# Performance work log

Hardware: AMD Instinct MI355X
Metric: run time of the kernel (lower is better)

The kernel has to match this reference:

```python
import jax, jax.numpy as jnp
import numpy as np

IN_FEATURES = 256
N_HEADS = 4
N_HIDDEN = 128  # out_features, concat=False
SLOPE = 0.1
NEG_INF = -9e15


def setup_inputs() -> dict:
    key = jax.random.key(0)
    k1, k2, k3, k4 = jax.random.split(key, 4)
    N = 8192
    h = jax.random.normal(k1, (N, IN_FEATURES), dtype=jnp.float32)
    adj_mat = jax.random.randint(k2, (N, N), 0, 2, dtype=jnp.int32)
    # xavier_normal with gain=1.414
    std_W = 1.414 * (2.0 / (IN_FEATURES + N_HIDDEN * N_HEADS)) ** 0.5
    W = jax.random.normal(k3, (IN_FEATURES, N_HIDDEN * N_HEADS), dtype=jnp.float32) * std_W
    std_a = 1.414 * (2.0 / (2 * N_HIDDEN + 1)) ** 0.5
    a = jax.random.normal(k4, (N_HEADS, 2 * N_HIDDEN, 1), dtype=jnp.float32) * std_a
    return {"h": h, "adj_mat": adj_mat, "W": W, "a": a}


def reference(h, adj_mat, W, a):
    N = h.shape[0]
    # linear projection -> [H, N, d]
    ht = (h @ W).reshape(N, N_HEADS, N_HIDDEN).transpose(1, 0, 2)
    # dropout is identity (eval / p effectively 0), then LeakyReLU
    ht = jnp.where(ht >= 0, ht, SLOPE * ht)
    # additive attention scores: src[h,i] + tgt[h,j]
    src = jnp.einsum('hnd,hd->hn', ht, a[:, :N_HIDDEN, 0])  # [H, N]
    tgt = jnp.einsum('hnd,hd->hn', ht, a[:, N_HIDDEN:, 0])  # [H, N]
    e = src[:, :, None] + tgt[:, None, :]                   # [H, N, N]
    e = jnp.where(adj_mat[None, :, :] > 0, e, NEG_INF)
    attn = jax.nn.softmax(e, axis=-1)
    # weighted sum and mean over heads (concat=False)
    out = jnp.einsum('hnm,hmd->hnd', attn, ht).mean(axis=0)  # [N, d]
    return out
```

## Files before the change

kernel.cpp:

```cpp
#include <hip/hip_runtime.h>


typedef unsigned short u16;
typedef unsigned int u32;
using bf16x8 = __attribute__((ext_vector_type(8))) short;
using f32x4  = __attribute__((ext_vector_type(4))) float;

typedef const void __attribute__((address_space(1))) gas_void;
typedef void __attribute__((address_space(3))) las_void;
#define GLD16(g, l) __builtin_amdgcn_global_load_lds((gas_void*)(g), (las_void*)(l), 16, 0, 0)

__device__ __forceinline__ u16 f2bf(float f) {
  u32 u = __float_as_uint(f);
  return (u16)((u + 0x7FFFu + ((u >> 16) & 1u)) >> 16);
}
__device__ __forceinline__ float bf2f(u16 u) {
  return __uint_as_float(((u32)u) << 16);
}

__global__ void transpose_w(const float* __restrict__ W, float* __restrict__ Wt) {
  __shared__ float tile[32][33];
  int cb = blockIdx.x * 32, kb = blockIdx.y * 32;
  int tc = threadIdx.x & 31, tr = threadIdx.x >> 5;
  for (int p = 0; p < 32; p += 8)
    tile[tr + p][tc] = W[(size_t)(kb + tr + p) * 512 + cb + tc];
  __syncthreads();
  for (int p = 0; p < 32; p += 8)
    Wt[(size_t)(cb + tr + p) * 256 + kb + tc] = tile[tc][tr + p];
}

__global__ void ht_gemm(const float* __restrict__ h, const float* __restrict__ Wt,
                        u16* __restrict__ HT) {
  __shared__ __align__(16) u16 Abuf[128 * 40];
  __shared__ __align__(16) u16 Bbuf[128 * 40];
  int tid = threadIdx.x;
  int cb = blockIdx.x, rb = blockIdx.y;
  int r0 = rb * 128, c0 = cb * 128;
  int lane = tid & 63, wv = tid >> 6;
  int wr = wv >> 1, wc = wv & 1;
  int mrow = lane & 15, q = lane >> 4;
  int ch = tid & 7, m0 = tid >> 3;

  f32x4 acc[4][4];
#pragma unroll
  for (int i = 0; i < 4; i++)
#pragma unroll
    for (int j = 0; j < 4; j++) acc[i][j] = f32x4{0.f, 0.f, 0.f, 0.f};

  for (int kt = 0; kt < 256; kt += 32) {
    __syncthreads();
#pragma unroll
    for (int mp = 0; mp < 128; mp += 32) {
      int m = m0 + mp;
      float4 v = *(const float4*)(&h[(size_t)(r0 + m) * 256 + kt + ch * 4]);
      uint2 p;
      p.x = (u32)f2bf(v.x) | ((u32)f2bf(v.y) << 16);
      p.y = (u32)f2bf(v.z) | ((u32)f2bf(v.w) << 16);
      *(uint2*)(&Abuf[m * 40 + ch * 4]) = p;
      float4 u = *(const float4*)(&Wt[(size_t)(c0 + m) * 256 + kt + ch * 4]);
      uint2 r;
      r.x = (u32)f2bf(u.x) | ((u32)f2bf(u.y) << 16);
      r.y = (u32)f2bf(u.z) | ((u32)f2bf(u.w) << 16);
      *(uint2*)(&Bbuf[m * 40 + ch * 4]) = r;
    }
    __syncthreads();
    bf16x8 af[4], bfv[4];
#pragma unroll
    for (int i = 0; i < 4; i++)
      af[i] = *(const bf16x8*)(&Abuf[(wr * 64 + i * 16 + mrow) * 40 + q * 8]);
#pragma unroll
    for (int j = 0; j < 4; j++)
      bfv[j] = *(const bf16x8*)(&Bbuf[(wc * 64 + j * 16 + mrow) * 40 + q * 8]);
#pragma unroll
    for (int i = 0; i < 4; i++)
#pragma unroll
      for (int j = 0; j < 4; j++)
        acc[i][j] = __builtin_amdgcn_mfma_f32_16x16x32_bf16(af[i], bfv[j], acc[i][j], 0, 0, 0);
  }
#pragma unroll
  for (int i = 0; i < 4; i++)
#pragma unroll
    for (int j = 0; j < 4; j++)
#pragma unroll
      for (int r = 0; r < 4; r++) {
        int gi = r0 + wr * 64 + i * 16 + q * 4 + r;
        int gc = c0 + wc * 64 + j * 16 + mrow;
        float v = acc[i][j][r];
        v = v >= 0.f ? v : 0.1f * v;
        HT[(size_t)gi * 512 + gc] = f2bf(v);
      }
}

__global__ void build_yt(const u16* __restrict__ HT, const float* __restrict__ a,
                         u16* __restrict__ Yt) {
  __shared__ u16 sht[64][528];
  __shared__ float swv[64 * 4];
  __shared__ float sa[512];
  int t = threadIdx.x;
  int j0 = blockIdx.x * 64;
  for (int i = t; i < 512; i += 256) {
    int g = i >> 7, d = i & 127;
    sa[i] = a[g * 256 + 128 + d];
  }
#pragma unroll
  for (int p = 0; p < 16; ++p) {
    int el = t + 256 * p;
    int row = el >> 6, col8 = el & 63;
    *(uint4*)(&sht[row][col8 * 8]) = *(const uint4*)(&HT[(size_t)(j0 + row) * 512 + col8 * 8]);
  }
  __syncthreads();
  {
    int jl = t >> 2, g = t & 3;
    float acc = 0.f;
#pragma unroll
    for (int d8 = 0; d8 < 16; ++d8) {
      bf16x8 v = *(const bf16x8*)(&sht[jl][g * 128 + d8 * 8]);
#pragma unroll
      for (int u = 0; u < 8; ++u)
        acc += bf2f((u16)v[u]) * sa[g * 128 + d8 * 8 + u];
    }
    swv[jl * 4 + g] = __expf(acc);
  }
  __syncthreads();
  int oj = (t & 7) * 8, oc = t >> 3;
  for (int pass = 0; pass < 17; ++pass) {
    int c = pass * 32 + oc;
    if (c >= 528) break;
    u32 pk[4] = {0u, 0u, 0u, 0u};
    if (c < 512) {
      int g = c >> 7;
#pragma unroll
      for (int u = 0; u < 4; ++u) {
        int j = oj + 2 * u;
        float v0 = bf2f(sht[j][c]) * swv[j * 4 + g];
        float v1 = bf2f(sht[j + 1][c]) * swv[(j + 1) * 4 + g];
        pk[u] = (u32)f2bf(v0) | ((u32)f2bf(v1) << 16);
      }
    } else if (c < 516) {
      int g = c - 512;
#pragma unroll
      for (int u = 0; u < 4; ++u) {
        int j = oj + 2 * u;
        float v0 = swv[j * 4 + g];
        float v1 = swv[(j + 1) * 4 + g];
        pk[u] = (u32)f2bf(v0) | ((u32)f2bf(v1) << 16);
      }
    }
    *(uint4*)(&Yt[(size_t)c * 8192 + j0 + oj]) = make_uint4(pk[0], pk[1], pk[2], pk[3]);
  }
}

__global__ __launch_bounds__(256, 2) void adj_gemm(const int* __restrict__ adj,
                                                   const u16* __restrict__ Yt,
                                                   float* __restrict__ C,
                                                   float* __restrict__ S) {
  __shared__ __align__(16) u16 Abuf[2][64 * 32];
  __shared__ __align__(16) u16 Bbuf[2][512 * 32];
  __shared__ __align__(16) u16 Bden[2][16 * 32];
  int tid = threadIdx.x;
  int rb = blockIdx.x, kh = blockIdx.y;
  int r0 = rb * 64, k0 = kh * 2048;
  int lane = tid & 63, wv = tid >> 6;
  int mrow = lane & 15, q = lane >> 4;
  int qs = q ^ ((mrow >> 1) & 3);
  int am = tid >> 2, aq = tid & 3;
  int asw = am * 32 + ((aq ^ ((am >> 1) & 3)) * 8);
  const int* aptr = &adj[(size_t)(r0 + am) * 8192 + k0 + aq * 8];
  int brow = lane >> 2;
  int bq = (lane & 3) ^ ((lane >> 3) & 3);

  f32x4 acc[4][8];
#pragma unroll
  for (int i = 0; i < 4; i++)
#pragma unroll
    for (int j = 0; j < 8; j++) acc[i][j] = f32x4{0.f, 0.f, 0.f, 0.f};
  f32x4 accD[4];
#pragma unroll
  for (int i = 0; i < 4; i++) accD[i] = f32x4{0.f, 0.f, 0.f, 0.f};

  {
#pragma unroll
    for (int p = 0; p < 8; ++p)
      GLD16(&Yt[(size_t)(wv * 128 + p * 16 + brow) * 8192 + k0 + bq * 8],
            &Bbuf[0][(wv * 128 + p * 16) * 32]);
    if (wv == 0)
      GLD16(&Yt[(size_t)(512 + brow) * 8192 + k0 + bq * 8], &Bden[0][0]);
    int4 v0 = *(const int4*)(aptr);
    int4 v1 = *(const int4*)(aptr + 4);
    uint4 pk;
    pk.x = 16256u * ((u32)v0.x | ((u32)v0.y << 16));
    pk.y = 16256u * ((u32)v0.z | ((u32)v0.w << 16));
    pk.z = 16256u * ((u32)v1.x | ((u32)v1.y << 16));
    pk.w = 16256u * ((u32)v1.z | ((u32)v1.w << 16));
    *(uint4*)(&Abuf[0][asw]) = pk;
    __syncthreads();
  }

  int cur = 0;
  for (int t = 0; t < 63; ++t) {
    int nxt = cur ^ 1;
    int kt = k0 + (t + 1) * 32;
#pragma unroll
    for (int p = 0; p < 8; ++p)
      GLD16(&Yt[(size_t)(wv * 128 + p * 16 + brow) * 8192 + kt + bq * 8],
            &Bbuf[nxt][(wv * 128 + p * 16) * 32]);
    if (wv == 0)
      GLD16(&Yt[(size_t)(512 + brow) * 8192 + kt + bq * 8], &Bden[nxt][0]);
    const int* ap = aptr + (size_t)(t + 1) * 32;
    int4 v0 = *(const int4*)(ap);
    int4 v1 = *(const int4*)(ap + 4);
    bf16x8 af[4], bfv[8];
#pragma unroll
    for (int i = 0; i < 4; i++)
      af[i] = *(const bf16x8*)(&Abuf[cur][(i * 16 + mrow) * 32 + qs * 8]);
#pragma unroll
    for (int j = 0; j < 8; j++)
      bfv[j] = *(const bf16x8*)(&Bbuf[cur][(wv * 128 + j * 16 + mrow) * 32 + qs * 8]);
#pragma unroll
    for (int i = 0; i < 4; i++)
#pragma unroll
      for (int j = 0; j < 8; j++)
        acc[i][j] = __builtin_amdgcn_mfma_f32_16x16x32_bf16(af[i], bfv[j], acc[i][j], 0, 0, 0);
    if (wv == 0) {
      bf16x8 bd = *(const bf16x8*)(&Bden[cur][mrow * 32 + qs * 8]);
#pragma unroll
      for (int i = 0; i < 4; i++)
        accD[i] = __builtin_amdgcn_mfma_f32_16x16x32_bf16(af[i], bd, accD[i], 0, 0, 0);
    }
    uint4 pk;
    pk.x = 16256u * ((u32)v0.x | ((u32)v0.y << 16));
    pk.y = 16256u * ((u32)v0.z | ((u32)v0.w << 16));
    pk.z = 16256u * ((u32)v1.x | ((u32)v1.y << 16));
    pk.w = 16256u * ((u32)v1.z | ((u32)v1.w << 16));
    *(uint4*)(&Abuf[nxt][asw]) = pk;
    __syncthreads();
    cur = nxt;
  }
  {
    bf16x8 af[4], bfv[8];
#pragma unroll
    for (int i = 0; i < 4; i++)
      af[i] = *(const bf16x8*)(&Abuf[cur][(i * 16 + mrow) * 32 + qs * 8]);
#pragma unroll
    for (int j = 0; j < 8; j++)
      bfv[j] = *(const bf16x8*)(&Bbuf[cur][(wv * 128 + j * 16 + mrow) * 32 + qs * 8]);
#pragma unroll
    for (int i = 0; i < 4; i++)
#pragma unroll
      for (int j = 0; j < 8; j++)
        acc[i][j] = __builtin_amdgcn_mfma_f32_16x16x32_bf16(af[i], bfv[j], acc[i][j], 0, 0, 0);
    if (wv == 0) {
      bf16x8 bd = *(const bf16x8*)(&Bden[cur][mrow * 32 + qs * 8]);
#pragma unroll
      for (int i = 0; i < 4; i++)
        accD[i] = __builtin_amdgcn_mfma_f32_16x16x32_bf16(af[i], bd, accD[i], 0, 0, 0);
    }
  }

  float* Ck = C + (size_t)kh * 8192 * 512;
#pragma unroll
  for (int i = 0; i < 4; i++)
#pragma unroll
    for (int j = 0; j < 8; j++)
#pragma unroll
      for (int r = 0; r < 4; r++) {
        int gi = r0 + i * 16 + q * 4 + r;
        int gc = wv * 128 + j * 16 + mrow;
        Ck[(size_t)gi * 512 + gc] = acc[i][j][r];
      }
  if (wv == 0 && mrow < 4) {
    float* Sk = S + (size_t)kh * 4 * 8192;
#pragma unroll
    for (int i = 0; i < 4; i++)
#pragma unroll
      for (int r = 0; r < 4; r++) {
        int gi = r0 + i * 16 + q * 4 + r;
        Sk[(size_t)mrow * 8192 + gi] = accD[i][r];
      }
  }
}

__global__ void finalize_gat(const float* __restrict__ C, const float* __restrict__ S,
                             float* __restrict__ out) {
  int idx = blockIdx.x * 256 + threadIdx.x;
  int i = idx >> 7, d = idx & 127;
  float s = 0.f;
#pragma unroll
  for (int g = 0; g < 4; ++g) {
    float num = 0.f, den = 0.f;
#pragma unroll
    for (int kh = 0; kh < 4; ++kh) {
      num += C[(size_t)kh * 8192 * 512 + (size_t)i * 512 + g * 128 + d];
      den += S[(size_t)kh * 4 * 8192 + (size_t)g * 8192 + i];
    }
    s += num / den;
  }
  out[idx] = 0.25f * s;
}

extern "C" void kernel_launch(void* const* d_in, const int* in_sizes, int n_in,
                              void* d_out, int out_size, void* d_ws, size_t ws_size,
                              hipStream_t stream) {
  const float* h   = (const float*)d_in[0];
  const int*   adj = (const int*)d_in[1];
  const float* W   = (const float*)d_in[2];
  const float* a   = (const float*)d_in[3];
  float* out = (float*)d_out;
  char* ws = (char*)d_ws;
  float* Wt = (float*)(ws + 0);
  u16*   HT = (u16*)(ws + 524288);
  u16*   Yt = (u16*)(ws + 8912896);
  float* C  = (float*)(ws + 17563648);
  float* S  = (float*)(ws + 84672512);

  transpose_w<<<dim3(16, 8), 256, 0, stream>>>(W, Wt);
  ht_gemm<<<dim3(4, 64), 256, 0, stream>>>(h, Wt, HT);
  build_yt<<<dim3(128), 256, 0, stream>>>(HT, a, Yt);
  adj_gemm<<<dim3(128, 4), 256, 0, stream>>>(adj, Yt, C, S);
  finalize_gat<<<dim3(4096), 256, 0, stream>>>(C, S, out);
}
```

Before: 509.1 us.

## Load GEMM B operand directly from global into registers, bypassing LDS staging

The adj_gemm kernel no longer stages the Yt B tiles and the denominator tile in double-buffered LDS through global_load_lds. Each wave now loads its own B fragments straight from global memory into registers, since no other wave reads them. Only the adjacency A tile stays in LDS, and the __syncthreads is replaced by an lgkmcnt wait plus s_barrier, so the barrier no longer waits on outstanding vector memory loads. This removes about 66KB of LDS per block and the LDS write/read round trip. In exchange, global load latency is no longer hidden by a one-tile-ahead prefetch, and the strided 64-byte row reads may coalesce less well.

Result: slower. 527.4 us (+3.6%).

```diff
diff --git a/kernel.cpp b/kernel.cpp
--- a/kernel.cpp
+++ b/kernel.cpp
@@ -5,10 +5,6 @@
 typedef unsigned int u32;
 using bf16x8 = __attribute__((ext_vector_type(8))) short;
 using f32x4  = __attribute__((ext_vector_type(4))) float;
-
-typedef const void __attribute__((address_space(1))) gas_void;
-typedef void __attribute__((address_space(3))) las_void;
-#define GLD16(g, l) __builtin_amdgcn_global_load_lds((gas_void*)(g), (las_void*)(l), 16, 0, 0)
 
 __device__ __forceinline__ u16 f2bf(float f) {
   u32 u = __float_as_uint(f);
@@ -155,8 +151,6 @@
                                                    float* __restrict__ C,
                                                    float* __restrict__ S) {
   __shared__ __align__(16) u16 Abuf[2][64 * 32];
-  __shared__ __align__(16) u16 Bbuf[2][512 * 32];
-  __shared__ __align__(16) u16 Bden[2][16 * 32];
   int tid = threadIdx.x;
   int rb = blockIdx.x, kh = blockIdx.y;
   int r0 = rb * 64, k0 = kh * 2048;
@@ -166,8 +160,8 @@
   int am = tid >> 2, aq = tid & 3;
   int asw = am * 32 + ((aq ^ ((am >> 1) & 3)) * 8);
   const int* aptr = &adj[(size_t)(r0 + am) * 8192 + k0 + aq * 8];
-  int brow = lane >> 2;
-  int bq = (lane & 3) ^ ((lane >> 3) & 3);
+  const u16* bbase = &Yt[(size_t)(wv * 128 + mrow) * 8192 + k0 + q * 8];
+  const u16* dbase = &Yt[(size_t)(512 + mrow) * 8192 + k0 + q * 8];
 
   f32x4 acc[4][8];
 #pragma unroll
@@ -179,12 +173,6 @@
   for (int i = 0; i < 4; i++) accD[i] = f32x4{0.f, 0.f, 0.f, 0.f};
 
   {
-#pragma unroll
-    for (int p = 0; p < 8; ++p)
-      GLD16(&Yt[(size_t)(wv * 128 + p * 16 + brow) * 8192 + k0 + bq * 8],
-            &Bbuf[0][(wv * 128 + p * 16) * 32]);
-    if (wv == 0)
-      GLD16(&Yt[(size_t)(512 + brow) * 8192 + k0 + bq * 8], &Bden[0][0]);
     int4 v0 = *(const int4*)(aptr);
     int4 v1 = *(const int4*)(aptr + 4);
     uint4 pk;
@@ -193,68 +181,49 @@
     pk.z = 16256u * ((u32)v1.x | ((u32)v1.y << 16));
     pk.w = 16256u * ((u32)v1.z | ((u32)v1.w << 16));
     *(uint4*)(&Abuf[0][asw]) = pk;
-    __syncthreads();
-  }
-
-  int cur = 0;
-  for (int t = 0; t < 63; ++t) {
-    int nxt = cur ^ 1;
-    int kt = k0 + (t + 1) * 32;
-#pragma unroll
-    for (int p = 0; p < 8; ++p)
-      GLD16(&Yt[(size_t)(wv * 128 + p * 16 + brow) * 8192 + kt + bq * 8],
-            &Bbuf[nxt][(wv * 128 + p * 16) * 32]);
-    if (wv == 0)
-      GLD16(&Yt[(size_t)(512 + brow) * 8192 + kt + bq * 8], &Bden[nxt][0]);
-    const int* ap = aptr + (size_t)(t + 1) * 32;
-    int4 v0 = *(const int4*)(ap);
-    int4 v1 = *(const int4*)(ap + 4);
-    bf16x8 af[4], bfv[8];
+  }
+  asm volatile("s_waitcnt lgkmcnt(0)" ::: "memory");
+  __builtin_amdgcn_s_barrier();
+
+  for (int t = 0; t < 64; ++t) {
+    int cur = t & 1;
+    size_t koff = (size_t)t * 32;
+    bf16x8 bfv[8];
+#pragma unroll
+    for (int j = 0; j < 8; j++)
+      bfv[j] = *(const bf16x8*)(bbase + (size_t)j * 16 * 8192 + koff);
+    bf16x8 bd;
+    if (wv == 0) bd = *(const bf16x8*)(dbase + koff);
+    int4 v0, v1;
+    if (t < 63) {
+      const int* ap = aptr + (size_t)(t + 1) * 32;
+      v0 = *(const int4*)(ap);
+      v1 = *(const int4*)(ap + 4);
+    }
+    bf16x8 af[4];
 #pragma unroll
     for (int i = 0; i < 4; i++)
       af[i] = *(const bf16x8*)(&Abuf[cur][(i * 16 + mrow) * 32 + qs * 8]);
 #pragma unroll
     for (int j = 0; j < 8; j++)
-      bfv[j] = *(const bf16x8*)(&Bbuf[cur][(wv * 128 + j * 16 + mrow) * 32 + qs * 8]);
-#pragma unroll
-    for (int i = 0; i < 4; i++)
-#pragma unroll
-      for (int j = 0; j < 8; j++)
+#pragma unroll
+      for (int i = 0; i < 4; i++)
         acc[i][j] = __builtin_amdgcn_mfma_f32_16x16x32_bf16(af[i], bfv[j], acc[i][j], 0, 0, 0);
     if (wv == 0) {
-      bf16x8 bd = *(const bf16x8*)(&Bden[cur][mrow * 32 + qs * 8]);
 #pragma unroll
       for (int i = 0; i < 4; i++)
         accD[i] = __builtin_amdgcn_mfma_f32_16x16x32_bf16(af[i], bd, accD[i], 0, 0, 0);
     }
-    uint4 pk;
-    pk.x = 16256u * ((u32)v0.x | ((u32)v0.y << 16));
-    pk.y = 16256u * ((u32)v0.z | ((u32)v0.w << 16));
-    pk.z = 16256u * ((u32)v1.x | ((u32)v1.y << 16));
-    pk.w = 16256u * ((u32)v1.z | ((u32)v1.w << 16));
-    *(uint4*)(&Abuf[nxt][asw]) = pk;
-    __syncthreads();
-    cur = nxt;
-  }
-  {
-    bf16x8 af[4], bfv[8];
-#pragma unroll
-    for (int i = 0; i < 4; i++)
-      af[i] = *(const bf16x8*)(&Abuf[cur][(i * 16 + mrow) * 32 + qs * 8]);
-#pragma unroll
-    for (int j = 0; j < 8; j++)
-      bfv[j] = *(const bf16x8*)(&Bbuf[cur][(wv * 128 + j * 16 + mrow) * 32 + qs * 8]);
-#pragma unroll
-    for (int i = 0; i < 4; i++)
-#pragma unroll
-      for (int j = 0; j < 8; j++)
-        acc[i][j] = __builtin_amdgcn_mfma_f32_16x16x32_bf16(af[i], bfv[j], acc[i][j], 0, 0, 0);
-    if (wv == 0) {
-      bf16x8 bd = *(const bf16x8*)(&Bden[cur][mrow * 32 + qs * 8]);
-#pragma unroll
-      for (int i = 0; i < 4; i++)
-        accD[i] = __builtin_amdgcn_mfma_f32_16x16x32_bf16(af[i], bd, accD[i], 0, 0, 0);
-    }
+    if (t < 63) {
+      uint4 pk;
+      pk.x = 16256u * ((u32)v0.x | ((u32)v0.y << 16));
+      pk.y = 16256u * ((u32)v0.z | ((u32)v0.w << 16));
+      pk.z = 16256u * ((u32)v1.x | ((u32)v1.y << 16));
+      pk.w = 16256u * ((u32)v1.z | ((u32)v1.w << 16));
+      *(uint4*)(&Abuf[cur ^ 1][asw]) = pk;
+    }
+    asm volatile("s_waitcnt lgkmcnt(0)" ::: "memory");
+    __builtin_amdgcn_s_barrier();
   }
 
   float* Ck = C + (size_t)kh * 8192 * 512;
```
